# Kernel tuning notes

Measured on AMD Instinct MI355X. Metric: run time of the kernel, lower is better.

Reference implementation:

```python
import math
import jax, jax.numpy as jnp
import numpy as np

B, C, E = 8, 2048, 1024

def setup_inputs() -> dict:
    key = jax.random.key(0)
    ks = jax.random.split(key, 7)
    s_e = 1.0 / math.sqrt(E)
    s_c = 1.0 / math.sqrt(C)
    return {
        'x': jax.random.normal(ks[0], (B, C, E), dtype=jnp.float32),
        'fc_w': jax.random.normal(ks[1], (E, E), dtype=jnp.float32) * s_e,
        'fc_b': jax.random.normal(ks[2], (E,), dtype=jnp.float32) * s_e,
        'alt_fc_w': jax.random.normal(ks[3], (C, C), dtype=jnp.float32) * s_c,
        'alt_fc_b': jax.random.normal(ks[4], (C,), dtype=jnp.float32) * s_c,
        'vfc_w': jax.random.normal(ks[5], (E, E), dtype=jnp.float32) * s_e,
        'vfc_b': jax.random.normal(ks[6], (E,), dtype=jnp.float32) * s_e,
    }

def reference(x, fc_w, fc_b, alt_fc_w, alt_fc_b, vfc_w, vfc_b):
    # y = fc(x): [b,c,e]
    y = jnp.einsum('bce,fe->bcf', x, fc_w) + fc_b
    # yx = alt_fc(x^T): [b,e,c] -> Linear over context dim -> [b,e,k]
    xx = jnp.swapaxes(x, 1, 2)                    # [b,e,c]
    yx = jnp.einsum('bec,kc->bek', xx, alt_fc_w) + alt_fc_b
    # attention scores: [b,c,k]
    attn = jnp.einsum('bce,bek->bck', y, yx)
    scale = 1.0 / math.sqrt(attn.shape[-1])
    attn = jax.nn.softmax(attn * scale, axis=-1)
    # values
    vx = jnp.einsum('bke,fe->bkf', x, vfc_w) + vfc_b
    out = jnp.einsum('bck,bke->bce', attn, vx)
    # post_feed=None -> return y only
    return out
```

## Files before the change

### kernel.cpp

```cpp
#include <hip/hip_runtime.h>
#include <stdint.h>

#define Bb 8
#define Cc 2048
#define Ee 1024

typedef unsigned short u16;
typedef __attribute__((ext_vector_type(8))) short short8;
typedef __attribute__((ext_vector_type(4))) float f32x4;

__device__ __forceinline__ u16 f2bf(float f){
    unsigned u = __builtin_bit_cast(unsigned, f);
    return (u16)((u + 0x7fffu + ((u >> 16) & 1u)) >> 16);
}
__device__ __forceinline__ float bf2f(u16 h){
    return __builtin_bit_cast(float, ((unsigned)h) << 16);
}
__device__ __forceinline__ void gld16(const void* g, void* l){
    __builtin_amdgcn_global_load_lds(
        (const __attribute__((address_space(1))) unsigned int*)g,
        (__attribute__((address_space(3))) unsigned int*)l,
        16, 0, 0);
}
#define MFMA(a,b,c) __builtin_amdgcn_mfma_f32_16x16x32_bf16((a),(b),(c),0,0,0)
#define SBAR()  __builtin_amdgcn_s_barrier()
#define SCHED0() __builtin_amdgcn_sched_barrier(0)
#define LGKM8() asm volatile("s_waitcnt lgkmcnt(8)" ::: "memory")
#define LGKM4() asm volatile("s_waitcnt lgkmcnt(4)" ::: "memory")
#define LGKM0() asm volatile("s_waitcnt lgkmcnt(0)" ::: "memory")
#define VMCNT0() asm volatile("s_waitcnt vmcnt(0)" ::: "memory")

__global__ __launch_bounds__(256) void k_cast(const float* __restrict__ s,
                                              u16* __restrict__ d, long n4){
    long i = (long)blockIdx.x * 256 + threadIdx.x;
    const long stride = (long)gridDim.x * 256;
    for (; i < n4; i += stride){
        float4 f = ((const float4*)s)[i];
        ushort4 o = make_ushort4(f2bf(f.x), f2bf(f.y), f2bf(f.z), f2bf(f.w));
        ((ushort4*)d)[i] = o;
    }
}

__global__ __launch_bounds__(256) void k_cast_xt(const float* __restrict__ src,
                                                 u16* __restrict__ xb,
                                                 u16* __restrict__ xbT){
    __shared__ float tile[32][33];
    const int b = blockIdx.z;
    src += (long)b * Cc * Ee;
    xb  += (long)b * Cc * Ee;
    xbT += (long)b * Cc * Ee;
    const int c0 = blockIdx.x * 32;
    const int r0 = blockIdx.y * 32;
    const int tx = threadIdx.x & 31;
    const int ty = threadIdx.x >> 5;
    #pragma unroll
    for (int p = 0; p < 4; ++p){
        float v = src[(long)(r0 + ty + p*8) * Ee + c0 + tx];
        tile[ty + p*8][tx] = v;
        xb[(long)(r0 + ty + p*8) * Ee + c0 + tx] = f2bf(v);
    }
    __syncthreads();
    #pragma unroll
    for (int p = 0; p < 4; ++p)
        xbT[(long)(c0 + ty + p*8) * Cc + r0 + tx] = f2bf(tile[tx][ty + p*8]);
}

template<int BIAS_MODE, int OUT_F32>
__global__ __launch_bounds__(512, 2)
void k_gemm256(const u16* __restrict__ A, const u16* __restrict__ Bm,
               void* __restrict__ Cout, const float* __restrict__ bias,
               int N, int K, long sA, long sB, long sC, float scale)
{
    __shared__ __attribute__((aligned(16))) char smem[131072];

    const int gx = gridDim.x, gy = gridDim.y;
    const int nwg = gx * gy * gridDim.z;
    const int lin = blockIdx.x + gx * (blockIdx.y + gy * blockIdx.z);
    const int swz = (lin & 7) * (nwg >> 3) + (lin >> 3);
    const int bx = swz % gx;
    const int tmp = swz / gx;
    const int by = tmp % gy;
    const int bz = tmp / gy;

    A  += (long)bz * sA;
    Bm += (long)bz * sB;
    u16*   Cm = (u16*)Cout + (OUT_F32 ? 0 : (long)bz * sC);
    float* Cf = (float*)Cout + (OUT_F32 ? (long)bz * sC : 0);

    const int tid  = threadIdx.x;
    const int lane = tid & 63;
    const int wave = tid >> 6;
    const int wr = wave >> 2;
    const int wc = wave & 3;
    const int tileM = bx * 256;
    const int tileN = by * 256;

    const int srow   = tid >> 3;
    const int schunk = (tid & 7) ^ (srow & 7);
    const u16* Ag = A  + (long)(tileM + srow) * K + schunk * 8;
    const u16* Bg = Bm + (long)(tileN + srow) * K + schunk * 8;
    const long uK = (long)64 * K;
    const int  ldst = tid * 16;

    const int lrow = lane & 15;
    const int lk   = lane >> 4;
    const int sw   = lrow & 7;
    const int cs0  = ((0 + lk) ^ sw) * 16;
    const int cs1  = ((4 + lk) ^ sw) * 16;
    const int arow0 = (wr*128 + lrow) * 128;
    const int brow0 = 32768 + (wc*64 + lrow) * 128;

    f32x4 acc[8][4];
    #pragma unroll
    for (int m = 0; m < 8; ++m)
        #pragma unroll
        for (int n = 0; n < 4; ++n)
            acc[m][n] = (f32x4){0.f,0.f,0.f,0.f};

    char* sm = smem;
    #pragma unroll
    for (int u = 0; u < 4; ++u) gld16(Bg + u*uK, sm + 32768 + u*8192 + ldst);
    #pragma unroll
    for (int u = 0; u < 4; ++u) gld16(Ag + u*uK, sm + u*8192 + ldst);
    __syncthreads();

    const int NT = K >> 6;
    short8 aA[4], aB[4], bK0[4], bK1[4];

    for (int t = 0; t < NT; ++t){
        const bool pref = (t + 1) < NT;
        char* cbuf = sm + ((t & 1) << 16);
        char* nbuf = sm + (((t + 1) & 1) << 16);
        const u16* Agt = Ag + (long)(t + 1) * 64;
        const u16* Bgt = Bg + (long)(t + 1) * 64;

        if (pref){
            gld16(Agt + 0*uK, nbuf + 0*8192 + ldst);
            gld16(Agt + 1*uK, nbuf + 1*8192 + ldst);
            gld16(Agt + 2*uK, nbuf + 2*8192 + ldst);
            gld16(Agt + 3*uK, nbuf + 3*8192 + ldst);
            gld16(Bgt + 0*uK, nbuf + 32768 + 0*8192 + ldst);
            gld16(Bgt + 1*uK, nbuf + 32768 + 1*8192 + ldst);
            gld16(Bgt + 2*uK, nbuf + 32768 + 2*8192 + ldst);
            gld16(Bgt + 3*uK, nbuf + 32768 + 3*8192 + ldst);
        }

        #pragma unroll
        for (int m = 0; m < 4; ++m) aA[m]  = *(const short8*)(cbuf + arow0 + m*2048 + cs0);
        #pragma unroll
        for (int n = 0; n < 4; ++n) bK0[n] = *(const short8*)(cbuf + brow0 + n*2048 + cs0);
        #pragma unroll
        for (int m = 0; m < 4; ++m) aB[m]  = *(const short8*)(cbuf + arow0 + m*2048 + cs1);
        #pragma unroll
        for (int n = 0; n < 4; ++n) bK1[n] = *(const short8*)(cbuf + brow0 + n*2048 + cs1);

        LGKM8(); SCHED0();
        __builtin_amdgcn_s_setprio(1);
        #pragma unroll
        for (int m = 0; m < 4; ++m)
            #pragma unroll
            for (int n = 0; n < 4; ++n)
                acc[m][n] = MFMA(aA[m], bK0[n], acc[m][n]);
        __builtin_amdgcn_s_setprio(0);

        #pragma unroll
        for (int m = 0; m < 4; ++m) aA[m] = *(const short8*)(cbuf + arow0 + (m+4)*2048 + cs0);
        LGKM4(); SCHED0();
        __builtin_amdgcn_s_setprio(1);
        #pragma unroll
        for (int m = 0; m < 4; ++m)
            #pragma unroll
            for (int n = 0; n < 4; ++n)
                acc[m][n] = MFMA(aB[m], bK1[n], acc[m][n]);
        __builtin_amdgcn_s_setprio(0);

        #pragma unroll
        for (int m = 0; m < 4; ++m) aB[m] = *(const short8*)(cbuf + arow0 + (m+4)*2048 + cs1);
        LGKM4(); SCHED0();
        __builtin_amdgcn_s_setprio(1);
        #pragma unroll
        for (int m = 0; m < 4; ++m)
            #pragma unroll
            for (int n = 0; n < 4; ++n)
                acc[m+4][n] = MFMA(aA[m], bK0[n], acc[m+4][n]);
        __builtin_amdgcn_s_setprio(0);

        LGKM0(); SCHED0();
        __builtin_amdgcn_s_setprio(1);
        #pragma unroll
        for (int m = 0; m < 4; ++m)
            #pragma unroll
            for (int n = 0; n < 4; ++n)
                acc[m+4][n] = MFMA(aB[m], bK1[n], acc[m+4][n]);
        __builtin_amdgcn_s_setprio(0);

        VMCNT0(); SBAR(); SCHED0();
    }

    const int r0base = tileM + wr*128 + lk*4;
    const int cbase  = tileN + wc*64 + lrow;
    #pragma unroll
    for (int m = 0; m < 8; ++m){
        const int r0 = r0base + m*16;
        #pragma unroll
        for (int n = 0; n < 4; ++n){
            const int c = cbase + n*16;
            f32x4 v = acc[m][n];
            #pragma unroll
            for (int j = 0; j < 4; ++j){
                float val = v[j] * scale;
                if (BIAS_MODE == 1) val += bias[c];
                if (BIAS_MODE == 2) val += bias[r0 + j];
                if (OUT_F32) Cf[(long)(r0 + j) * N + c] = val;
                else         Cm[(long)(r0 + j) * N + c] = f2bf(val);
            }
        }
    }
}

__global__ __launch_bounds__(256) void k_softmax(u16* __restrict__ P){
    u16* p = P + (long)blockIdx.x * Cc;
    const int tid = threadIdx.x;
    short8 raw = *(const short8*)(p + tid * 8);
    float v[8];
    float mx = -3.0e38f;
    #pragma unroll
    for (int i = 0; i < 8; ++i){ v[i] = bf2f((u16)raw[i]); mx = fmaxf(mx, v[i]); }
    #pragma unroll
    for (int o = 32; o > 0; o >>= 1) mx = fmaxf(mx, __shfl_xor(mx, o));
    __shared__ float redm[4];
    if ((tid & 63) == 0) redm[tid >> 6] = mx;
    __syncthreads();
    mx = fmaxf(fmaxf(redm[0], redm[1]), fmaxf(redm[2], redm[3]));
    float s = 0.f;
    #pragma unroll
    for (int i = 0; i < 8; ++i){ v[i] = __expf(v[i] - mx); s += v[i]; }
    #pragma unroll
    for (int o = 32; o > 0; o >>= 1) s += __shfl_xor(s, o);
    __shared__ float reds[4];
    if ((tid & 63) == 0) reds[tid >> 6] = s;
    __syncthreads();
    s = reds[0] + reds[1] + reds[2] + reds[3];
    const float inv = 1.f / s;
    short8 o8;
    #pragma unroll
    for (int i = 0; i < 8; ++i) o8[i] = (short)f2bf(v[i] * inv);
    *(short8*)(p + tid * 8) = o8;
}

static inline int cast_grid(long n4){
    long g = (n4 + 255) / 256;
    return (int)(g > 2048 ? 2048 : g);
}

extern "C" void kernel_launch(void* const* d_in, const int* in_sizes, int n_in,
                              void* d_out, int out_size, void* d_ws, size_t ws_size,
                              hipStream_t stream)
{
    const float* x     = (const float*)d_in[0];
    const float* fc_w  = (const float*)d_in[1];
    const float* fc_b  = (const float*)d_in[2];
    const float* altw  = (const float*)d_in[3];
    const float* altb  = (const float*)d_in[4];
    const float* vfc_w = (const float*)d_in[5];
    const float* vfc_b = (const float*)d_in[6];
    float* out = (float*)d_out;

    char* ws = (char*)d_ws;
    const size_t nBCE = (size_t)Bb * Cc * Ee;
    u16* xb   = (u16*)(ws);
    u16* xbT  = (u16*)(ws + 2 * nBCE);
    u16* P    = (u16*)(ws);
    u16* y    = (u16*)(ws + 4 * nBCE);
    u16* z    = (u16*)(ws + 6 * nBCE);
    u16* vxT  = (u16*)(ws + 8 * nBCE);
    u16* fcwb = (u16*)(ws + 10 * nBCE);
    u16* vfwb = fcwb + (size_t)Ee * Ee;
    u16* awb  = vfwb + (size_t)Ee * Ee;

    k_cast_xt<<<dim3(Ee / 32, Cc / 32, Bb), 256, 0, stream>>>(x, xb, xbT);
    k_cast<<<cast_grid((long)Ee * Ee / 4), 256, 0, stream>>>(fc_w, fcwb, (long)Ee * Ee / 4);
    k_cast<<<cast_grid((long)Ee * Ee / 4), 256, 0, stream>>>(vfc_w, vfwb, (long)Ee * Ee / 4);
    k_cast<<<cast_grid((long)Cc * Cc / 4), 256, 0, stream>>>(altw, awb, (long)Cc * Cc / 4);

    const long sBCE = (long)Cc * Ee;
    const long sBCC = (long)Cc * Cc;
    dim3 blk(512);

    k_gemm256<1, 0><<<dim3(Cc/256, Ee/256, Bb), blk, 0, stream>>>(
        xb, fcwb, y, fc_b, Ee, Ee, sBCE, 0, sBCE, 1.f);

    k_gemm256<2, 0><<<dim3(Ee/256, Cc/256, Bb), blk, 0, stream>>>(
        vfwb, xb, vxT, vfc_b, Cc, Ee, 0, sBCE, sBCE, 1.f);

    k_gemm256<2, 0><<<dim3(Cc/256, Ee/256, Bb), blk, 0, stream>>>(
        awb, xbT, z, altb, Ee, Cc, 0, sBCE, sBCE, 1.f);

    k_gemm256<0, 0><<<dim3(Cc/256, Cc/256, Bb), blk, 0, stream>>>(
        y, z, P, nullptr, Cc, Ee, sBCE, sBCE, sBCC, 0.022097086912079608f);

    k_softmax<<<Bb * Cc, 256, 0, stream>>>(P);

    k_gemm256<0, 1><<<dim3(Cc/256, Ee/256, Bb), blk, 0, stream>>>(
        P, vxT, out, nullptr, Ee, Cc, sBCC, sBCE, sBCE, 1.f);
}
```

Baseline: 340.6 us.

## Split GEMM K-tile staging into half-tiles with finer-grained vmcnt pipelining

Restructures the bf16 MFMA GEMM main loop so each 64-wide K tile is staged as two 32-wide halves, with a new LDS layout of 64-byte rows and a 4-way XOR swizzle. Global-to-LDS loads for the next halves are issued between MFMA groups, and partial vmcnt waits replace the full vmcnt(0) drain at the end of every tile. This is meant to overlap global loads with compute and avoid stalling on all outstanding loads each iteration. In exchange it adds more barriers per tile, a more complex schedule, and assumes NT is even.

```diff
diff --git a/kernel.cpp b/kernel.cpp
--- a/kernel.cpp
+++ b/kernel.cpp
@@ -28,6 +28,8 @@
 #define LGKM8() asm volatile("s_waitcnt lgkmcnt(8)" ::: "memory")
 #define LGKM4() asm volatile("s_waitcnt lgkmcnt(4)" ::: "memory")
 #define LGKM0() asm volatile("s_waitcnt lgkmcnt(0)" ::: "memory")
+#define VMCNT8() asm volatile("s_waitcnt vmcnt(8)" ::: "memory")
+#define VMCNT6() asm volatile("s_waitcnt vmcnt(6)" ::: "memory")
 #define VMCNT0() asm volatile("s_waitcnt vmcnt(0)" ::: "memory")
 
 __global__ __launch_bounds__(256) void k_cast(const float* __restrict__ s,
@@ -95,20 +97,23 @@
     const int tileM = bx * 256;
     const int tileN = by * 256;
 
-    const int srow   = tid >> 3;
-    const int schunk = (tid & 7) ^ (srow & 7);
-    const u16* Ag = A  + (long)(tileM + srow) * K + schunk * 8;
-    const u16* Bg = Bm + (long)(tileN + srow) * K + schunk * 8;
-    const long uK = (long)64 * K;
+    const int srow = tid >> 2;
+    const int schk = (tid & 3) ^ (srow & 3);
+    const u16* Ag = A  + (long)(tileM + srow) * K + schk * 8;
+    const u16* Bg = Bm + (long)(tileN + srow) * K + schk * 8;
+    const long rk128 = (long)128 * K;
     const int  ldst = tid * 16;
+
+    #define STGA(tt,j) { gld16(Ag + (long)(tt)*64 + (j)*32,         smem + ((tt)&1)*32768 + (j)*16384 + ldst); \
+                         gld16(Ag + (long)(tt)*64 + (j)*32 + rk128, smem + ((tt)&1)*32768 + (j)*16384 + 8192 + ldst); }
+    #define STGB(tt,j) { gld16(Bg + (long)(tt)*64 + (j)*32,         smem + 65536 + ((tt)&1)*32768 + (j)*16384 + ldst); \
+                         gld16(Bg + (long)(tt)*64 + (j)*32 + rk128, smem + 65536 + ((tt)&1)*32768 + (j)*16384 + 8192 + ldst); }
 
     const int lrow = lane & 15;
     const int lk   = lane >> 4;
-    const int sw   = lrow & 7;
-    const int cs0  = ((0 + lk) ^ sw) * 16;
-    const int cs1  = ((4 + lk) ^ sw) * 16;
-    const int arow0 = (wr*128 + lrow) * 128;
-    const int brow0 = 32768 + (wc*64 + lrow) * 128;
+    const int cs   = (lk ^ (lrow & 3)) << 4;
+    const int arow = (wr*128 + lrow) * 64;
+    const int brow = 65536 + (wc*64 + lrow) * 64;
 
     f32x4 acc[8][4];
     #pragma unroll
@@ -117,84 +122,86 @@
         for (int n = 0; n < 4; ++n)
             acc[m][n] = (f32x4){0.f,0.f,0.f,0.f};
 
-    char* sm = smem;
-    #pragma unroll
-    for (int u = 0; u < 4; ++u) gld16(Bg + u*uK, sm + 32768 + u*8192 + ldst);
-    #pragma unroll
-    for (int u = 0; u < 4; ++u) gld16(Ag + u*uK, sm + u*8192 + ldst);
-    __syncthreads();
-
     const int NT = K >> 6;
-    short8 aA[4], aB[4], bK0[4], bK1[4];
-
-    for (int t = 0; t < NT; ++t){
-        const bool pref = (t + 1) < NT;
-        char* cbuf = sm + ((t & 1) << 16);
-        char* nbuf = sm + (((t + 1) & 1) << 16);
-        const u16* Agt = Ag + (long)(t + 1) * 64;
-        const u16* Bgt = Bg + (long)(t + 1) * 64;
-
-        if (pref){
-            gld16(Agt + 0*uK, nbuf + 0*8192 + ldst);
-            gld16(Agt + 1*uK, nbuf + 1*8192 + ldst);
-            gld16(Agt + 2*uK, nbuf + 2*8192 + ldst);
-            gld16(Agt + 3*uK, nbuf + 3*8192 + ldst);
-            gld16(Bgt + 0*uK, nbuf + 32768 + 0*8192 + ldst);
-            gld16(Bgt + 1*uK, nbuf + 32768 + 1*8192 + ldst);
-            gld16(Bgt + 2*uK, nbuf + 32768 + 2*8192 + ldst);
-            gld16(Bgt + 3*uK, nbuf + 32768 + 3*8192 + ldst);
-        }
-
-        #pragma unroll
-        for (int m = 0; m < 4; ++m) aA[m]  = *(const short8*)(cbuf + arow0 + m*2048 + cs0);
-        #pragma unroll
-        for (int n = 0; n < 4; ++n) bK0[n] = *(const short8*)(cbuf + brow0 + n*2048 + cs0);
-        #pragma unroll
-        for (int m = 0; m < 4; ++m) aB[m]  = *(const short8*)(cbuf + arow0 + m*2048 + cs1);
-        #pragma unroll
-        for (int n = 0; n < 4; ++n) bK1[n] = *(const short8*)(cbuf + brow0 + n*2048 + cs1);
-
+    short8 aE[4], aO[4], bE[4], bO[4];
+
+    STGA(0,0); STGB(0,0); STGA(0,1); STGB(0,1); STGA(1,0); STGB(1,0);
+    VMCNT8(); SBAR(); SCHED0();
+    #pragma unroll
+    for (int m = 0; m < 4; ++m) aE[m] = *(const short8*)(smem + arow + m*1024 + cs);
+    #pragma unroll
+    for (int n = 0; n < 4; ++n) bE[n] = *(const short8*)(smem + brow + n*1024 + cs);
+
+    auto tile_body = [&](int t, int ab, int nb) __attribute__((always_inline)) {
+        const bool g1 = (t + 1) < NT;
+        const bool g2 = (t + 2) < NT;
+        const bool dr = t >= NT - 2;
+
+        #pragma unroll
+        for (int m = 0; m < 4; ++m) aO[m] = *(const short8*)(smem + ab + arow + (m+4)*1024 + cs);
+        if (g1) STGA(t+1, 1);
+        LGKM4(); SCHED0();
+        __builtin_amdgcn_s_setprio(1);
+        #pragma unroll
+        for (int m = 0; m < 4; ++m)
+            #pragma unroll
+            for (int n = 0; n < 4; ++n)
+                acc[m][n] = MFMA(aE[m], bE[n], acc[m][n]);
+        __builtin_amdgcn_s_setprio(0);
+        if (dr) { VMCNT0(); } else { VMCNT6(); }
+        SBAR(); SCHED0();
+
+        #pragma unroll
+        for (int m = 0; m < 4; ++m) aE[m] = *(const short8*)(smem + ab + 16384 + arow + m*1024 + cs);
+        #pragma unroll
+        for (int n = 0; n < 4; ++n) bO[n] = *(const short8*)(smem + ab + 16384 + brow + n*1024 + cs);
+        if (g1) STGB(t+1, 1);
         LGKM8(); SCHED0();
         __builtin_amdgcn_s_setprio(1);
         #pragma unroll
         for (int m = 0; m < 4; ++m)
             #pragma unroll
             for (int n = 0; n < 4; ++n)
-                acc[m][n] = MFMA(aA[m], bK0[n], acc[m][n]);
+                acc[m+4][n] = MFMA(aO[m], bE[n], acc[m+4][n]);
         __builtin_amdgcn_s_setprio(0);
-
-        #pragma unroll
-        for (int m = 0; m < 4; ++m) aA[m] = *(const short8*)(cbuf + arow0 + (m+4)*2048 + cs0);
+        SBAR(); SCHED0();
+
+        #pragma unroll
+        for (int m = 0; m < 4; ++m) aO[m] = *(const short8*)(smem + ab + 16384 + arow + (m+4)*1024 + cs);
+        if (g2) STGA(t+2, 0);
         LGKM4(); SCHED0();
         __builtin_amdgcn_s_setprio(1);
         #pragma unroll
         for (int m = 0; m < 4; ++m)
             #pragma unroll
             for (int n = 0; n < 4; ++n)
-                acc[m][n] = MFMA(aB[m], bK1[n], acc[m][n]);
+                acc[m][n] = MFMA(aE[m], bO[n], acc[m][n]);
         __builtin_amdgcn_s_setprio(0);
-
-        #pragma unroll
-        for (int m = 0; m < 4; ++m) aB[m] = *(const short8*)(cbuf + arow0 + (m+4)*2048 + cs1);
-        LGKM4(); SCHED0();
+        if (dr) { VMCNT0(); } else { VMCNT6(); }
+        SBAR(); SCHED0();
+
+        if (g1){
+            #pragma unroll
+            for (int m = 0; m < 4; ++m) aE[m] = *(const short8*)(smem + nb + arow + m*1024 + cs);
+            #pragma unroll
+            for (int n = 0; n < 4; ++n) bE[n] = *(const short8*)(smem + nb + brow + n*1024 + cs);
+        }
+        if (g2) STGB(t+2, 0);
+        if (g1) { LGKM8(); } else { LGKM0(); }
+        SCHED0();
         __builtin_amdgcn_s_setprio(1);
         #pragma unroll
         for (int m = 0; m < 4; ++m)
             #pragma unroll
             for (int n = 0; n < 4; ++n)
-                acc[m+4][n] = MFMA(aA[m], bK0[n], acc[m+4][n]);
+                acc[m+4][n] = MFMA(aO[m], bO[n], acc[m+4][n]);
         __builtin_amdgcn_s_setprio(0);
-
-        LGKM0(); SCHED0();
-        __builtin_amdgcn_s_setprio(1);
-        #pragma unroll
-        for (int m = 0; m < 4; ++m)
-            #pragma unroll
-            for (int n = 0; n < 4; ++n)
-                acc[m+4][n] = MFMA(aB[m], bK1[n], acc[m+4][n]);
-        __builtin_amdgcn_s_setprio(0);
-
-        VMCNT0(); SBAR(); SCHED0();
+        SBAR(); SCHED0();
+    };
+
+    for (int t = 0; t < NT; t += 2){
+        tile_body(t,     0,     32768);
+        tile_body(t + 1, 32768, 0);
     }
 
     const int r0base = tileM + wr*128 + lk*4;
@@ -216,6 +223,8 @@
             }
         }
     }
+    #undef STGA
+    #undef STGB
 }
 
 __global__ __launch_bounds__(256) void k_softmax(u16* __restrict__ P){
```

Result: slower. 541.1 us (+58.9%).
